# Performance work log

Measured on AMD Instinct MI355X. Metric: run time of the kernel, lower is better.

## Reference

```python
import jax, jax.numpy as jnp
import numpy as np

HIDDEN = 4096
INTER = 16384
EPS = 1e-5


def setup_inputs() -> dict:
    key = jax.random.key(0)
    ks = jax.random.split(key, 10)
    B, S = 4, 2048
    inp = {
        'input': jax.random.normal(ks[0], (B, S, HIDDEN), jnp.float32),
        'residual': jax.random.normal(ks[1], (B, S, HIDDEN), jnp.float32),
        'residual_norm': jax.random.normal(ks[2], (B, S, HIDDEN), jnp.float32),
        'bias': jax.random.normal(ks[3], (HIDDEN,), jnp.float32) * 0.02,
        'attn_nw': jnp.ones((HIDDEN,), jnp.float32) + jax.random.normal(ks[4], (HIDDEN,), jnp.float32) * 0.02,
        'attn_nb': jax.random.normal(ks[5], (HIDDEN,), jnp.float32) * 0.02,
        'inter_w': jax.random.normal(ks[6], (HIDDEN, INTER), jnp.float32) * (1.0 / np.sqrt(HIDDEN)),
        'inter_b': jax.random.normal(ks[7], (INTER,), jnp.float32) * 0.02,
        'output_w': jax.random.normal(ks[8], (INTER, HIDDEN), jnp.float32) * (1.0 / np.sqrt(INTER)),
        'output_b': jax.random.normal(ks[9], (HIDDEN,), jnp.float32) * 0.02,
    }
    return inp


def _layernorm(x, gamma, beta, eps):
    mu = jnp.mean(x, axis=-1, keepdims=True)
    var = jnp.mean(jnp.square(x - mu), axis=-1, keepdims=True)
    return (x - mu) * jax.lax.rsqrt(var + eps) * gamma + beta


def reference(input, residual, residual_norm, bias, attn_nw, attn_nb,
              inter_w, inter_b, output_w, output_b):
    # pre_layer_norm + mlp_after_attn fp32 path of DeepSpeedMLP:
    # mlp_gemm: residual_add = input + residual + attn_bias; LN; GEMM+bias+GELU
    res = input + residual + bias                      # [B,S,H] attention residual add
    ln = _layernorm(res, attn_nw, attn_nb, EPS)
    inter = jax.nn.gelu(jnp.einsum('bsh,hi->bsi', ln, inter_w) + inter_b,
                        approximate=True)              # [B,S,I]
    out = jnp.einsum('bsi,ih->bsh', inter, output_w)   # vector_matmul
    # residual_add kernel (pre_layer_norm, mp_size=1): add residual path + mlp bias
    return out + res + output_b
```

## Files before the change

kernel.cpp:

```cpp
#include <hip/hip_runtime.h>
#include <hip/hip_bf16.h>
#include <cstdint>
#include <cstddef>

#define HIDDEN 4096
#define INTER  16384
#define NTOK   8192
#define LN_EPS 1e-5f

typedef unsigned short u16;
typedef u16   u16x8 __attribute__((ext_vector_type(8)));
typedef __bf16 bf16x8 __attribute__((ext_vector_type(8)));
typedef float  f32x4 __attribute__((ext_vector_type(4)));

__device__ __forceinline__ u16 f2bf(float f) {
    union { float f; unsigned int ui; } x;
    x.f = f;
    unsigned int u = x.ui;
    return (u16)((u + 0x7FFFu + ((u >> 16) & 1u)) >> 16);
}

__device__ __forceinline__ void gl_lds16(const u16* g, u16* l) {
    __builtin_amdgcn_global_load_lds(
        (const __attribute__((address_space(1))) void*)g,
        (__attribute__((address_space(3))) void*)l,
        16, 0, 0);
}

#define TDIM 64
__global__ __launch_bounds__(256) void cvt_transpose(const float* __restrict__ in,
                                                     u16* __restrict__ out,
                                                     int K, int N) {
    __shared__ float tile[TDIM][TDIM + 1];
    const int bn = blockIdx.x * TDIM;
    const int bk = blockIdx.y * TDIM;
    const int t  = threadIdx.x;
#pragma unroll
    for (int it = 0; it < 4; ++it) {
        int idx = it * 256 + t;
        int r = idx >> 4;
        int c = (idx & 15) * 4;
        const float4 v = *(const float4*)(in + (size_t)(bk + r) * N + bn + c);
        tile[r][c]     = v.x;
        tile[r][c + 1] = v.y;
        tile[r][c + 2] = v.z;
        tile[r][c + 3] = v.w;
    }
    __syncthreads();
#pragma unroll
    for (int it = 0; it < 2; ++it) {
        int idx = it * 256 + t;
        int r = idx >> 3;
        int c = (idx & 7) * 8;
        u16x8 o;
#pragma unroll
        for (int j = 0; j < 8; ++j) o[j] = f2bf(tile[c + j][r]);
        *(u16x8*)(out + (size_t)(bn + r) * K + bk + c) = o;
    }
}

__global__ __launch_bounds__(256) void fused_add_ln(const float* __restrict__ in,
                                                    const float* __restrict__ resid,
                                                    const float* __restrict__ bias,
                                                    const float* __restrict__ gamma,
                                                    const float* __restrict__ beta,
                                                    u16* __restrict__ out) {
    const int row = blockIdx.x;
    const size_t base = (size_t)row * HIDDEN;
    const int t = threadIdx.x;
    const int c0 = t * 16;
    float v[16];
    float s = 0.f, s2 = 0.f;
#pragma unroll
    for (int g = 0; g < 4; ++g) {
        float4 vi = *(const float4*)(in    + base + c0 + g * 4);
        float4 vr = *(const float4*)(resid + base + c0 + g * 4);
        float4 vb = *(const float4*)(bias  + c0 + g * 4);
        float xs[4] = {vi.x + vr.x + vb.x, vi.y + vr.y + vb.y,
                       vi.z + vr.z + vb.z, vi.w + vr.w + vb.w};
#pragma unroll
        for (int j = 0; j < 4; ++j) {
            float x = xs[j];
            v[g * 4 + j] = x;
            s += x;
            s2 += x * x;
        }
    }
#pragma unroll
    for (int off = 32; off > 0; off >>= 1) {
        s  += __shfl_down(s, off, 64);
        s2 += __shfl_down(s2, off, 64);
    }
    __shared__ float sred[4], s2red[4], stats[2];
    const int wave = t >> 6, lane = t & 63;
    if (lane == 0) { sred[wave] = s; s2red[wave] = s2; }
    __syncthreads();
    if (t == 0) {
        float ts  = sred[0] + sred[1] + sred[2] + sred[3];
        float ts2 = s2red[0] + s2red[1] + s2red[2] + s2red[3];
        float mean = ts * (1.0f / HIDDEN);
        float var  = ts2 * (1.0f / HIDDEN) - mean * mean;
        stats[0] = mean;
        stats[1] = rsqrtf(var + LN_EPS);
    }
    __syncthreads();
    const float mean = stats[0], rstd = stats[1];
#pragma unroll
    for (int g = 0; g < 2; ++g) {
        u16x8 o;
#pragma unroll
        for (int j = 0; j < 8; ++j) {
            int e = g * 8 + j;
            float gm = gamma[c0 + e];
            float bt = beta[c0 + e];
            o[j] = f2bf((v[e] - mean) * rstd * gm + bt);
        }
        *(u16x8*)(out + base + c0 + g * 8) = o;
    }
}

template <int IH>
__device__ __forceinline__ void lda_t(bf16x8 (&af)[4][2], const u16* p0, int s0, int s1) {
#pragma unroll
    for (int ii = 0; ii < 4; ++ii) {
        const u16* p = p0 + (IH * 64 + ii * 16) * 64;
        af[ii][0] = *(const bf16x8*)(p + s0);
        af[ii][1] = *(const bf16x8*)(p + s1);
    }
}

template <int JH>
__device__ __forceinline__ void ldb_t(bf16x8 (&bf)[4][2], const u16* p0, int s0, int s1) {
#pragma unroll
    for (int jj = 0; jj < 2; ++jj) {
        const u16* p = p0 + (JH * 2 + jj) * 1024;
        bf[JH * 2 + jj][0] = *(const bf16x8*)(p + s0);
        bf[JH * 2 + jj][1] = *(const bf16x8*)(p + s1);
    }
}

template <int IH, int JH>
__device__ __forceinline__ void mfma_q(f32x4 (&acc)[8][4], const bf16x8 (&af)[4][2],
                                       const bf16x8 (&bf)[4][2]) {
#pragma unroll
    for (int ii = 0; ii < 4; ++ii)
#pragma unroll
        for (int jj = 0; jj < 2; ++jj)
#pragma unroll
            for (int kk = 0; kk < 2; ++kk)
                acc[IH * 4 + ii][JH * 2 + jj] = __builtin_amdgcn_mfma_f32_16x16x32_bf16(
                    af[ii][kk], bf[JH * 2 + jj][kk], acc[IH * 4 + ii][JH * 2 + jj], 0, 0, 0);
}

template <int EPI>
__global__ __launch_bounds__(512, 2) void gemm256(const u16* __restrict__ A,
                                                  const u16* __restrict__ BT,
                                                  u16* __restrict__ Cb,
                                                  float* __restrict__ Cf,
                                                  const float* __restrict__ b0f,
                                                  const float* __restrict__ b1f,
                                                  const float* __restrict__ in_f,
                                                  const float* __restrict__ res_f,
                                                  int M, int N, int K) {
    (void)M;
    extern __shared__ u16 lds[];
    const int t    = threadIdx.x;
    const int wave = t >> 6;
    const int lane = t & 63;
    const int l16  = lane & 15;
    const int quad = lane >> 4;
    const int xlow = l16 & 7;
    const int rl   = lane >> 3;
    const int scol = ((lane & 7) ^ rl) * 8;

    const int gx   = gridDim.x;
    const int nwg  = gx * gridDim.y;
    const int orig = blockIdx.y * gx + blockIdx.x;
    const int wg   = (orig & 7) * (nwg >> 3) + (orig >> 3);
    const int m0   = (wg / gx) * 256;
    const int n0   = (wg % gx) * 256;

    const int wm = (wave >> 2) * 128;
    const int wn = (wave & 3) * 64;

    u16* const as0 = lds;
    u16* const bs0 = lds + 32768;

    const u16* pA = A  + (size_t)(m0 + wave * 16 + rl) * K + scol;
    const u16* pB = BT + (size_t)(n0 + wave * 16 + rl) * K + scol;

    const int aoff = (wm + l16) * 64;
    const int boff = (wn + l16) * 64;
    const int s0   = (quad ^ xlow) * 8;
    const int s1   = s0 ^ 32;

    auto stage = [&](const u16* pbase, int hh, int kcol, u16* ldst) {
#pragma unroll
        for (int call = 0; call < 2; ++call)
            gl_lds16(pbase + (size_t)(hh * 128 + call * 8) * (size_t)K + kcol,
                     ldst + hh * 8192 + (wave * 2 + call) * 512);
    };

    f32x4 acc[8][4];
#pragma unroll
    for (int i = 0; i < 8; ++i)
#pragma unroll
        for (int j = 0; j < 4; ++j)
            acc[i][j] = f32x4{0.f, 0.f, 0.f, 0.f};

    const int NT = K >> 6;

    stage(pA, 0, 0, as0);
    stage(pA, 1, 0, as0);
    stage(pB, 0, 0, bs0);
    stage(pB, 1, 0, bs0);
    if (NT > 1) {
        stage(pB, 0, 64, bs0 + 16384);
        stage(pB, 1, 64, bs0 + 16384);
        asm volatile("s_waitcnt vmcnt(4)" ::: "memory");
    } else {
        asm volatile("s_waitcnt vmcnt(0)" ::: "memory");
    }
    __builtin_amdgcn_s_barrier();

    bf16x8 af[4][2], bfv[4][2];

    for (int kt = 0; kt < NT; ++kt) {
        const int buf  = kt & 1;
        const u16* as_ = as0 + buf * 16384;
        const u16* bs_ = bs0 + buf * 16384;
        u16* an = as0 + (buf ^ 1) * 16384;
        u16* bw = bs0 + buf * 16384;
        const int  kcA = (kt + 1) << 6;
        const int  kcB = (kt + 2) << 6;
        const bool stA = (kt + 1 < NT);
        const bool stB = (kt + 2 < NT);

        lda_t<0>(af, as_ + aoff, s0, s1);
        ldb_t<0>(bfv, bs_ + boff, s0, s1);
        if (stA) stage(pA, 0, kcA, an);
        __builtin_amdgcn_s_barrier();
        asm volatile("s_waitcnt lgkmcnt(0)" ::: "memory");
        __builtin_amdgcn_s_setprio(1);
        mfma_q<0, 0>(acc, af, bfv);
        __builtin_amdgcn_s_setprio(0);
        __builtin_amdgcn_s_barrier();

        ldb_t<1>(bfv, bs_ + boff, s0, s1);
        if (stA) stage(pA, 1, kcA, an);
        __builtin_amdgcn_s_barrier();
        asm volatile("s_waitcnt lgkmcnt(0)" ::: "memory");
        __builtin_amdgcn_s_setprio(1);
        mfma_q<0, 1>(acc, af, bfv);
        __builtin_amdgcn_s_setprio(0);
        __builtin_amdgcn_s_barrier();

        lda_t<1>(af, as_ + aoff, s0, s1);
        if (stB) stage(pB, 0, kcB, bw);
        __builtin_amdgcn_s_barrier();
        asm volatile("s_waitcnt lgkmcnt(0)" ::: "memory");
        __builtin_amdgcn_s_setprio(1);
        mfma_q<1, 1>(acc, af, bfv);
        __builtin_amdgcn_s_setprio(0);
        __builtin_amdgcn_s_barrier();

        if (stB) stage(pB, 1, kcB, bw);
        __builtin_amdgcn_s_barrier();
        __builtin_amdgcn_s_setprio(1);
        mfma_q<1, 0>(acc, af, bfv);
        __builtin_amdgcn_s_setprio(0);
        if (stB) asm volatile("s_waitcnt vmcnt(4)" ::: "memory");
        else     asm volatile("s_waitcnt vmcnt(0)" ::: "memory");
        __builtin_amdgcn_s_barrier();
    }

#pragma unroll
    for (int i = 0; i < 8; ++i) {
#pragma unroll
        for (int j = 0; j < 4; ++j) {
            const int col = n0 + wn + j * 16 + l16;
            float badd;
            if (EPI == 0) badd = b0f[col];
            else          badd = b0f[col] + b1f[col];
#pragma unroll
            for (int r = 0; r < 4; ++r) {
                const int rowi = m0 + wm + i * 16 + quad * 4 + r;
                float x = acc[i][j][r];
                if (EPI == 0) {
                    x += badd;
                    float u  = 0.7978845608f * (x + 0.044715f * x * x * x);
                    float sg = 1.0f / (1.0f + __expf(-2.0f * u));
                    Cb[(size_t)rowi * N + col] = f2bf(x * sg);
                } else {
                    const size_t off = (size_t)rowi * N + col;
                    Cf[off] = x + in_f[off] + res_f[off] + badd;
                }
            }
        }
    }
}

extern "C" void kernel_launch(void* const* d_in, const int* in_sizes, int n_in,
                              void* d_out, int out_size, void* d_ws, size_t ws_size,
                              hipStream_t stream) {
    const float* input    = (const float*)d_in[0];
    const float* residual = (const float*)d_in[1];
    const float* bias     = (const float*)d_in[3];
    const float* attn_nw  = (const float*)d_in[4];
    const float* attn_nb  = (const float*)d_in[5];
    const float* inter_w  = (const float*)d_in[6];
    const float* inter_b  = (const float*)d_in[7];
    const float* output_w = (const float*)d_in[8];
    const float* output_b = (const float*)d_in[9];
    float* out = (float*)d_out;

    char* ws = (char*)d_ws;
    u16* w1t   = (u16*)(ws);
    u16* w2t   = (u16*)(ws + 134217728);
    u16* ln    = (u16*)(ws + 268435456);
    u16* inter = (u16*)(ws + 335544320);

    static int once = [] {
        hipFuncSetAttribute(reinterpret_cast<const void*>(gemm256<0>),
                            hipFuncAttributeMaxDynamicSharedMemorySize, 131072);
        hipFuncSetAttribute(reinterpret_cast<const void*>(gemm256<1>),
                            hipFuncAttributeMaxDynamicSharedMemorySize, 131072);
        return 0;
    }();
    (void)once;

    cvt_transpose<<<dim3(INTER / TDIM, HIDDEN / TDIM), 256, 0, stream>>>(inter_w, w1t, HIDDEN, INTER);
    cvt_transpose<<<dim3(HIDDEN / TDIM, INTER / TDIM), 256, 0, stream>>>(output_w, w2t, INTER, HIDDEN);
    fused_add_ln<<<NTOK, 256, 0, stream>>>(input, residual, bias, attn_nw, attn_nb, ln);
    gemm256<0><<<dim3(INTER / 256, NTOK / 256), 512, 131072, stream>>>(
        ln, w1t, inter, nullptr, inter_b, nullptr, nullptr, nullptr, NTOK, INTER, HIDDEN);
    gemm256<1><<<dim3(HIDDEN / 256, NTOK / 256), 512, 131072, stream>>>(
        inter, w2t, nullptr, out, bias, output_b, input, residual, NTOK, HIDDEN, INTER);
}
```

Baseline: 2.720 ms.

## Prefetch A tile half two steps ahead and remap tiles to XCDs for first GEMM

```diff
diff --git a/kernel.cpp b/kernel.cpp
--- a/kernel.cpp
+++ b/kernel.cpp
@@ -175,10 +175,22 @@
 
     const int gx   = gridDim.x;
     const int nwg  = gx * gridDim.y;
+    const int cpx  = nwg >> 3;
     const int orig = blockIdx.y * gx + blockIdx.x;
-    const int wg   = (orig & 7) * (nwg >> 3) + (orig >> 3);
-    const int m0   = (wg / gx) * 256;
-    const int n0   = (wg % gx) * 256;
+    const int xcd  = orig & 7;
+    const int c    = orig >> 3;
+    int mi, ni;
+    const int mpc  = cpx / gx;
+    if (EPI == 0 && mpc * gx == cpx) {
+        mi = xcd * mpc + (c % mpc);
+        ni = c / mpc;
+    } else {
+        const int wg = xcd * cpx + c;
+        mi = wg / gx;
+        ni = wg % gx;
+    }
+    const int m0 = mi * 256;
+    const int n0 = ni * 256;
 
     const int wm = (wave >> 2) * 128;
     const int wn = (wave & 3) * 64;
@@ -217,7 +229,8 @@
     if (NT > 1) {
         stage(pB, 0, 64, bs0 + 16384);
         stage(pB, 1, 64, bs0 + 16384);
-        asm volatile("s_waitcnt vmcnt(4)" ::: "memory");
+        stage(pA, 0, 64, as0 + 16384);
+        asm volatile("s_waitcnt vmcnt(6)" ::: "memory");
     } else {
         asm volatile("s_waitcnt vmcnt(0)" ::: "memory");
     }
@@ -229,16 +242,17 @@
         const int buf  = kt & 1;
         const u16* as_ = as0 + buf * 16384;
         const u16* bs_ = bs0 + buf * 16384;
-        u16* an = as0 + (buf ^ 1) * 16384;
-        u16* bw = bs0 + buf * 16384;
-        const int  kcA = (kt + 1) << 6;
-        const int  kcB = (kt + 2) << 6;
-        const bool stA = (kt + 1 < NT);
-        const bool stB = (kt + 2 < NT);
+        u16* an1 = as0 + (buf ^ 1) * 16384;
+        u16* a2  = as0 + buf * 16384;
+        u16* b2  = bs0 + buf * 16384;
+        const int  kc1 = (kt + 1) << 6;
+        const int  kc2 = (kt + 2) << 6;
+        const bool st1 = (kt + 1 < NT);
+        const bool st2 = (kt + 2 < NT);
 
         lda_t<0>(af, as_ + aoff, s0, s1);
         ldb_t<0>(bfv, bs_ + boff, s0, s1);
-        if (stA) stage(pA, 0, kcA, an);
+        if (st1) stage(pA, 1, kc1, an1);
         __builtin_amdgcn_s_barrier();
         asm volatile("s_waitcnt lgkmcnt(0)" ::: "memory");
         __builtin_amdgcn_s_setprio(1);
@@ -247,7 +261,6 @@
         __builtin_amdgcn_s_barrier();
 
         ldb_t<1>(bfv, bs_ + boff, s0, s1);
-        if (stA) stage(pA, 1, kcA, an);
         __builtin_amdgcn_s_barrier();
         asm volatile("s_waitcnt lgkmcnt(0)" ::: "memory");
         __builtin_amdgcn_s_setprio(1);
@@ -256,7 +269,7 @@
         __builtin_amdgcn_s_barrier();
 
         lda_t<1>(af, as_ + aoff, s0, s1);
-        if (stB) stage(pB, 0, kcB, bw);
+        if (st2) stage(pB, 0, kc2, b2);
         __builtin_amdgcn_s_barrier();
         asm volatile("s_waitcnt lgkmcnt(0)" ::: "memory");
         __builtin_amdgcn_s_setprio(1);
@@ -264,13 +277,16 @@
         __builtin_amdgcn_s_setprio(0);
         __builtin_amdgcn_s_barrier();
 
-        if (stB) stage(pB, 1, kcB, bw);
+        if (st2) {
+            stage(pB, 1, kc2, b2);
+            stage(pA, 0, kc2, a2);
+        }
         __builtin_amdgcn_s_barrier();
         __builtin_amdgcn_s_setprio(1);
         mfma_q<1, 0>(acc, af, bfv);
         __builtin_amdgcn_s_setprio(0);
-        if (stB) asm volatile("s_waitcnt vmcnt(4)" ::: "memory");
-        else     asm volatile("s_waitcnt vmcnt(0)" ::: "memory");
+        if (st2)      asm volatile("s_waitcnt vmcnt(6)" ::: "memory");
+        else if (st1) asm volatile("s_waitcnt vmcnt(0)" ::: "memory");
         __builtin_amdgcn_s_barrier();
     }
 
```

Result: no change. 2.684 ms (-1.3%).
